# Optimization experiments

Hardware: AMD Instinct MI355X
Metric: run time of the kernel (lower is better)

The kernel has to match this reference:

```python
import jax, jax.numpy as jnp
import numpy as np

H = 64
NUM_LAYERS = 2


def _edge_norm(si, ti, n_s, n_t):
    # per-edge sqrt(deg_src * deg_tgt), degrees counted over this edge type
    ds = jnp.zeros((n_s,), jnp.float32).at[si].add(1.0)
    dt = jnp.zeros((n_t,), jnp.float32).at[ti].add(1.0)
    return jnp.sqrt(ds[si] * dt[ti])


def _light_conv(xd, edge_list, div):
    # gather -> per-edge normalize -> scatter-add per edge type, then mean over
    # incoming edge types and ReLU (applied twice in original since ReLU=True;
    # relu is idempotent)
    out = {}
    for (src, tgt, si, ti, norm) in edge_list:
        msg = xd[src][si] / norm[:, None]          # [E, H]
        agg = jnp.zeros_like(xd[tgt]).at[ti].add(msg)
        out[tgt] = out[tgt] + agg if tgt in out else agg
    return {k: jax.nn.relu(v / div[k]) for k, v in out.items()}


def _run_branch(x0, edge_list, div):
    # concat=True: mean over stacked per-layer outputs; initial embeddings are
    # included only for spot and user (as in the original forward)
    all_x = {k: [] for k in x0}
    all_x['spot'].append(x0['spot'])
    all_x['user'].append(x0['user'])
    xd = x0
    for _ in range(NUM_LAYERS):
        xd = _light_conv(xd, edge_list, div)
        for k in xd:
            all_x[k].append(xd[k])
    return {k: jnp.mean(jnp.stack(v, axis=1), axis=1) for k, v in all_x.items()}


def setup_inputs() -> dict:
    key = jax.random.key(0)
    ks = jax.random.split(key, 32)
    NU, NS, NC, NCI, NP = 200000, 50000, 512, 2000, 47
    E_US, E_SC, E_SCI, E_CP = 1000000, 50000, 50000, 2000

    def emb(k, n):
        return 0.1 * jax.random.normal(k, (n, H), dtype=jnp.float32)

    inp = {
        'user1': emb(ks[0], NU), 'spot1': emb(ks[1], NS),
        'user2': emb(ks[2], NU), 'spot2': emb(ks[3], NS), 'cat2': emb(ks[4], NC),
        'user3': emb(ks[5], NU), 'spot3': emb(ks[6], NS),
        'city3': emb(ks[7], NCI), 'pref3': emb(ks[8], NP),
        'user4': emb(ks[9], NU), 'spot4': emb(ks[10], NS),
        'city4': emb(ks[11], NCI), 'pref4': emb(ks[12], NP), 'cat4': emb(ks[13], NC),
        'lin_w_user': 0.0625 * jax.random.normal(ks[14], (4 * H, 1), jnp.float32),
        'lin_b_user': jnp.zeros((1,), jnp.float32),
        'lin_w_spot': 0.0625 * jax.random.normal(ks[15], (4 * H, 1), jnp.float32),
        'lin_b_spot': jnp.zeros((1,), jnp.float32),
        'us_src': jax.random.randint(ks[16], (E_US,), 0, NU, jnp.int32),
        'us_dst': jax.random.randint(ks[17], (E_US,), 0, NS, jnp.int32),
        'sc_src': jax.random.randint(ks[18], (E_SC,), 0, NS, jnp.int32),
        'sc_dst': jax.random.randint(ks[19], (E_SC,), 0, NC, jnp.int32),
        'sci_src': jax.random.randint(ks[20], (E_SCI,), 0, NS, jnp.int32),
        'sci_dst': jax.random.randint(ks[21], (E_SCI,), 0, NCI, jnp.int32),
        'cp_src': jax.random.randint(ks[22], (E_CP,), 0, NCI, jnp.int32),
        'cp_dst': jax.random.randint(ks[23], (E_CP,), 0, NP, jnp.int32),
    }
    return inp


def reference(user1, spot1, user2, spot2, cat2, user3, spot3, city3, pref3,
              user4, spot4, city4, pref4, cat4,
              lin_w_user, lin_b_user, lin_w_spot, lin_b_spot,
              us_src, us_dst, sc_src, sc_dst, sci_src, sci_dst, cp_src, cp_dst):
    NU, NS = user1.shape[0], spot1.shape[0]
    NC, NCI, NP = cat2.shape[0], city3.shape[0], pref3.shape[0]

    n_us = _edge_norm(us_src, us_dst, NU, NS)
    n_sc = _edge_norm(sc_src, sc_dst, NS, NC)
    n_sci = _edge_norm(sci_src, sci_dst, NS, NCI)
    n_cp = _edge_norm(cp_src, cp_dst, NCI, NP)

    us_f = ('user', 'spot', us_src, us_dst, n_us)
    us_r = ('spot', 'user', us_dst, us_src, n_us)
    sc_f = ('spot', 'category', sc_src, sc_dst, n_sc)
    sc_r = ('category', 'spot', sc_dst, sc_src, n_sc)
    sci_f = ('spot', 'city', sci_src, sci_dst, n_sci)
    sci_r = ('city', 'spot', sci_dst, sci_src, n_sci)
    cp_f = ('city', 'pref', cp_src, cp_dst, n_cp)
    cp_r = ('pref', 'city', cp_dst, cp_src, n_cp)

    b1 = _run_branch({'user': user1, 'spot': spot1},
                     [us_f, us_r], {'spot': 1.0, 'user': 1.0})
    b2 = _run_branch({'user': user2, 'spot': spot2, 'category': cat2},
                     [us_f, us_r, sc_f, sc_r],
                     {'spot': 2.0, 'user': 1.0, 'category': 1.0})
    b3 = _run_branch({'user': user3, 'spot': spot3, 'city': city3, 'pref': pref3},
                     [us_f, us_r, sci_f, sci_r, cp_f, cp_r],
                     {'spot': 2.0, 'user': 1.0, 'city': 2.0, 'pref': 1.0})
    b4 = _run_branch({'user': user4, 'spot': spot4, 'city': city4,
                      'pref': pref4, 'category': cat4},
                     [us_f, us_r, sc_f, sc_r, sci_f, sci_r, cp_f, cp_r],
                     {'spot': 3.0, 'user': 1.0, 'city': 2.0, 'pref': 1.0,
                      'category': 1.0})

    xu = jnp.concatenate([b1['user'], b2['user'], b3['user'], b4['user']], axis=1)
    xs = jnp.concatenate([b1['spot'], b2['spot'], b3['spot'], b4['spot']], axis=1)
    user_out = xu @ lin_w_user + lin_b_user   # [NU, 1]
    spot_out = xs @ lin_w_spot + lin_b_spot   # [NS, 1]
    return jnp.concatenate([user_out, spot_out], axis=0)
```

## Files before the change

### kernel.cpp

```cpp
#include <hip/hip_runtime.h>

#define HD 64
#define ROW 256

__device__ inline unsigned short f2bf(float f) {
    unsigned u = __builtin_bit_cast(unsigned, f);
    u += 0x7FFFu + ((u >> 16) & 1u);
    return (unsigned short)(u >> 16);
}
__device__ inline float bf2f(unsigned short h) {
    unsigned u = ((unsigned)h) << 16;
    return __builtin_bit_cast(float, u);
}


__global__ void k_count(const int* __restrict__ s, const int* __restrict__ t, int E,
                        unsigned* __restrict__ ds, unsigned* __restrict__ dt) {
    int i = blockIdx.x * blockDim.x + threadIdx.x;
    int st = gridDim.x * blockDim.x;
    for (; i < E; i += st) {
        atomicAdd(ds + s[i], 1u);
        atomicAdd(dt + t[i], 1u);
    }
}

__global__ void k_rs(const unsigned* __restrict__ d, float* __restrict__ r, int n) {
    int i = blockIdx.x * blockDim.x + threadIdx.x;
    if (i < n) {
        unsigned v = d[i];
        r[i] = v ? 1.0f / sqrtf((float)v) : 0.0f;
    }
}

__global__ void k_off(const unsigned* __restrict__ deg, int n, unsigned* __restrict__ off,
                      unsigned* __restrict__ cur, unsigned* __restrict__ cnt) {
    int i = blockIdx.x * blockDim.x + threadIdx.x;
    if (i < n) {
        unsigned o = atomicAdd(cnt, deg[i]);
        off[i] = o;
        cur[i] = o;
    }
}

__global__ void k_fill(const int* __restrict__ s, const int* __restrict__ t, int E,
                       unsigned* __restrict__ cur, int* __restrict__ col) {
    int i = blockIdx.x * blockDim.x + threadIdx.x;
    int st = gridDim.x * blockDim.x;
    for (; i < E; i += st) {
        int p = (int)atomicAdd(cur + t[i], 1u);
        col[p] = s[i];
    }
}

__global__ void k_sentinel(float* __restrict__ out, int n, float val) {
    int i = blockIdx.x * blockDim.x + threadIdx.x;
    if (i < n) out[i] = val;
}


__global__ void k_l1_user(const int* __restrict__ col, const unsigned* __restrict__ off,
                          const unsigned* __restrict__ deg,
                          const float* __restrict__ rs_src, const float* __restrict__ rs_dst,
                          const float* __restrict__ s1, const float* __restrict__ s2,
                          const float* __restrict__ s3, const float* __restrict__ s4,
                          unsigned short* __restrict__ out, int n) {
    int w = (blockIdx.x * blockDim.x + threadIdx.x) >> 6;
    int lane = threadIdx.x & 63;
    if (w >= n) return;
    unsigned o = off[w], d = deg[w];
    float a0 = 0, a1 = 0, a2 = 0, a3 = 0;
    for (unsigned e = 0; e < d; ++e) {
        int s = col[o + e];
        float sc = rs_src[s];
        int b = s * HD + lane;
        a0 = fmaf(s1[b], sc, a0);
        a1 = fmaf(s2[b], sc, a1);
        a2 = fmaf(s3[b], sc, a2);
        a3 = fmaf(s4[b], sc, a3);
    }
    float rd = rs_dst[w];
    ushort4 pk;
    pk.x = f2bf(fmaxf(a0 * rd, 0.f));
    pk.y = f2bf(fmaxf(a1 * rd, 0.f));
    pk.z = f2bf(fmaxf(a2 * rd, 0.f));
    pk.w = f2bf(fmaxf(a3 * rd, 0.f));
    *reinterpret_cast<ushort4*>(out + w * ROW + lane * 4) = pk;
}

__global__ void k_l1_spot(
    const int* __restrict__ colU, const unsigned* __restrict__ offU, const unsigned* __restrict__ degU,
    const float* __restrict__ rsU_src, const float* __restrict__ rsU_dst,
    const int* __restrict__ colC, const unsigned* __restrict__ offC, const unsigned* __restrict__ degC,
    const float* __restrict__ rsC_src, const float* __restrict__ rsC_dst,
    const int* __restrict__ colI, const unsigned* __restrict__ offI, const unsigned* __restrict__ degI,
    const float* __restrict__ rsI_src, const float* __restrict__ rsI_dst,
    const float* __restrict__ u1, const float* __restrict__ u2,
    const float* __restrict__ u3, const float* __restrict__ u4,
    const float* __restrict__ c2, const float* __restrict__ c4,
    const float* __restrict__ i3, const float* __restrict__ i4,
    unsigned short* __restrict__ out, int n) {
    int w = (blockIdx.x * blockDim.x + threadIdx.x) >> 6;
    int lane = threadIdx.x & 63;
    if (w >= n) return;
    float a0 = 0, a1 = 0, a2 = 0, a3 = 0;
    {
        unsigned o = offU[w], d = degU[w];
        for (unsigned e = 0; e < d; ++e) {
            int s = colU[o + e];
            float sc = rsU_src[s];
            int b = s * HD + lane;
            a0 = fmaf(u1[b], sc, a0);
            a1 = fmaf(u2[b], sc, a1);
            a2 = fmaf(u3[b], sc, a2);
            a3 = fmaf(u4[b], sc, a3);
        }
        float rd = rsU_dst[w];
        a0 *= rd; a1 *= rd; a2 *= rd; a3 *= rd;
    }
    float cA = 0, cB = 0;
    {
        unsigned o = offC[w], d = degC[w];
        for (unsigned e = 0; e < d; ++e) {
            int s = colC[o + e];
            float sc = rsC_src[s];
            int b = s * HD + lane;
            cA = fmaf(c2[b], sc, cA);
            cB = fmaf(c4[b], sc, cB);
        }
        float rd = rsC_dst[w];
        cA *= rd; cB *= rd;
    }
    float iA = 0, iB = 0;
    {
        unsigned o = offI[w], d = degI[w];
        for (unsigned e = 0; e < d; ++e) {
            int s = colI[o + e];
            float sc = rsI_src[s];
            int b = s * HD + lane;
            iA = fmaf(i3[b], sc, iA);
            iB = fmaf(i4[b], sc, iB);
        }
        float rd = rsI_dst[w];
        iA *= rd; iB *= rd;
    }
    ushort4 pk;
    pk.x = f2bf(fmaxf(a0, 0.f));
    pk.y = f2bf(fmaxf((a1 + cA) * 0.5f, 0.f));
    pk.z = f2bf(fmaxf((a2 + iA) * 0.5f, 0.f));
    pk.w = f2bf(fmaxf((a3 + cB + iB) * (1.0f / 3.0f), 0.f));
    *reinterpret_cast<ushort4*>(out + w * ROW + lane * 4) = pk;
}

__global__ void k_l1_cat(const int* __restrict__ col, const unsigned* __restrict__ off,
                         const unsigned* __restrict__ deg,
                         const float* __restrict__ rs_src, const float* __restrict__ rs_dst,
                         const float* __restrict__ s2, const float* __restrict__ s4,
                         unsigned short* __restrict__ out, int n) {
    int w = (blockIdx.x * blockDim.x + threadIdx.x) >> 6;
    int lane = threadIdx.x & 63;
    if (w >= n) return;
    unsigned o = off[w], d = deg[w];
    float a1 = 0, a3 = 0;
    for (unsigned e = 0; e < d; ++e) {
        int s = col[o + e];
        float sc = rs_src[s];
        int b = s * HD + lane;
        a1 = fmaf(s2[b], sc, a1);
        a3 = fmaf(s4[b], sc, a3);
    }
    float rd = rs_dst[w];
    ushort4 pk;
    pk.x = 0;
    pk.y = f2bf(fmaxf(a1 * rd, 0.f));
    pk.z = 0;
    pk.w = f2bf(fmaxf(a3 * rd, 0.f));
    *reinterpret_cast<ushort4*>(out + w * ROW + lane * 4) = pk;
}

__global__ void k_l1_city(const int* __restrict__ colS, const unsigned* __restrict__ offS,
                          const unsigned* __restrict__ degS,
                          const float* __restrict__ rsS_src, const float* __restrict__ rsS_dst,
                          const int* __restrict__ colP, const unsigned* __restrict__ offP,
                          const unsigned* __restrict__ degP,
                          const float* __restrict__ rsP_src, const float* __restrict__ rsP_dst,
                          const float* __restrict__ s3, const float* __restrict__ s4,
                          const float* __restrict__ p3, const float* __restrict__ p4,
                          unsigned short* __restrict__ out, int n) {
    int w = (blockIdx.x * blockDim.x + threadIdx.x) >> 6;
    int lane = threadIdx.x & 63;
    if (w >= n) return;
    float a2 = 0, a3 = 0;
    {
        unsigned o = offS[w], d = degS[w];
        for (unsigned e = 0; e < d; ++e) {
            int s = colS[o + e];
            float sc = rsS_src[s];
            int b = s * HD + lane;
            a2 = fmaf(s3[b], sc, a2);
            a3 = fmaf(s4[b], sc, a3);
        }
        float rd = rsS_dst[w];
        a2 *= rd; a3 *= rd;
    }
    float b2 = 0, b3 = 0;
    {
        unsigned o = offP[w], d = degP[w];
        for (unsigned e = 0; e < d; ++e) {
            int s = colP[o + e];
            float sc = rsP_src[s];
            int b = s * HD + lane;
            b2 = fmaf(p3[b], sc, b2);
            b3 = fmaf(p4[b], sc, b3);
        }
        float rd = rsP_dst[w];
        b2 *= rd; b3 *= rd;
    }
    ushort4 pk;
    pk.x = 0;
    pk.y = 0;
    pk.z = f2bf(fmaxf((a2 + b2) * 0.5f, 0.f));
    pk.w = f2bf(fmaxf((a3 + b3) * 0.5f, 0.f));
    *reinterpret_cast<ushort4*>(out + w * ROW + lane * 4) = pk;
}


__global__ void k_user_out(const int* __restrict__ col, const unsigned* __restrict__ off,
                           const unsigned* __restrict__ deg,
                           const float* __restrict__ rs_src, const float* __restrict__ rs_dst,
                           const unsigned short* __restrict__ l1spot,
                           const unsigned short* __restrict__ l1user,
                           const float* __restrict__ x1, const float* __restrict__ x2,
                           const float* __restrict__ x3, const float* __restrict__ x4,
                           const float* __restrict__ wlin, const float* __restrict__ blin,
                           float* __restrict__ out, int n) {
    int u = (blockIdx.x * blockDim.x + threadIdx.x) >> 6;
    int lane = threadIdx.x & 63;
    if (u >= n) return;
    float a0 = 0, a1 = 0, a2 = 0, a3 = 0;
    unsigned o = off[u], d = deg[u];
    for (unsigned e = 0; e < d; ++e) {
        int s = col[o + e];
        float sc = rs_src[s];
        ushort4 v = *reinterpret_cast<const ushort4*>(l1spot + s * ROW + lane * 4);
        a0 = fmaf(bf2f(v.x), sc, a0);
        a1 = fmaf(bf2f(v.y), sc, a1);
        a2 = fmaf(bf2f(v.z), sc, a2);
        a3 = fmaf(bf2f(v.w), sc, a3);
    }
    float rd = rs_dst[u];
    a0 = fmaxf(a0 * rd, 0.f);
    a1 = fmaxf(a1 * rd, 0.f);
    a2 = fmaxf(a2 * rd, 0.f);
    a3 = fmaxf(a3 * rd, 0.f);
    int xb = u * HD + lane;
    ushort4 lv = *reinterpret_cast<const ushort4*>(l1user + u * ROW + lane * 4);
    const float third = 1.0f / 3.0f;
    float m0 = (x1[xb] + bf2f(lv.x) + a0) * third;
    float m1 = (x2[xb] + bf2f(lv.y) + a1) * third;
    float m2 = (x3[xb] + bf2f(lv.z) + a2) * third;
    float m3 = (x4[xb] + bf2f(lv.w) + a3) * third;
    float p = m0 * wlin[lane] + m1 * wlin[HD + lane] + m2 * wlin[2 * HD + lane] +
              m3 * wlin[3 * HD + lane];
#pragma unroll
    for (int ofs = 32; ofs; ofs >>= 1) p += __shfl_xor(p, ofs, 64);
    if (lane == 0) out[u] = p + blin[0];
}

__global__ void k_spot_out(
    const int* __restrict__ colU, const unsigned* __restrict__ offU, const unsigned* __restrict__ degU,
    const float* __restrict__ rsU_src, const float* __restrict__ rsU_dst,
    const int* __restrict__ colC, const unsigned* __restrict__ offC, const unsigned* __restrict__ degC,
    const float* __restrict__ rsC_src, const float* __restrict__ rsC_dst,
    const int* __restrict__ colI, const unsigned* __restrict__ offI, const unsigned* __restrict__ degI,
    const float* __restrict__ rsI_src, const float* __restrict__ rsI_dst,
    const unsigned short* __restrict__ l1user, const unsigned short* __restrict__ l1cat,
    const unsigned short* __restrict__ l1city, const unsigned short* __restrict__ l1spot,
    const float* __restrict__ x1, const float* __restrict__ x2,
    const float* __restrict__ x3, const float* __restrict__ x4,
    const float* __restrict__ wlin, const float* __restrict__ blin,
    float* __restrict__ out, int n) {
    int w = (blockIdx.x * blockDim.x + threadIdx.x) >> 6;
    int lane = threadIdx.x & 63;
    if (w >= n) return;
    float a0 = 0, a1 = 0, a2 = 0, a3 = 0;
    {
        unsigned o = offU[w], d = degU[w];
        for (unsigned e = 0; e < d; ++e) {
            int s = colU[o + e];
            float sc = rsU_src[s];
            ushort4 v = *reinterpret_cast<const ushort4*>(l1user + s * ROW + lane * 4);
            a0 = fmaf(bf2f(v.x), sc, a0);
            a1 = fmaf(bf2f(v.y), sc, a1);
            a2 = fmaf(bf2f(v.z), sc, a2);
            a3 = fmaf(bf2f(v.w), sc, a3);
        }
        float rd = rsU_dst[w];
        a0 *= rd; a1 *= rd; a2 *= rd; a3 *= rd;
    }
    float cA = 0, cB = 0;
    {
        unsigned o = offC[w], d = degC[w];
        for (unsigned e = 0; e < d; ++e) {
            int s = colC[o + e];
            float sc = rsC_src[s];
            ushort4 v = *reinterpret_cast<const ushort4*>(l1cat + s * ROW + lane * 4);
            cA = fmaf(bf2f(v.y), sc, cA);
            cB = fmaf(bf2f(v.w), sc, cB);
        }
        float rd = rsC_dst[w];
        cA *= rd; cB *= rd;
    }
    float iA = 0, iB = 0;
    {
        unsigned o = offI[w], d = degI[w];
        for (unsigned e = 0; e < d; ++e) {
            int s = colI[o + e];
            float sc = rsI_src[s];
            ushort4 v = *reinterpret_cast<const ushort4*>(l1city + s * ROW + lane * 4);
            iA = fmaf(bf2f(v.z), sc, iA);
            iB = fmaf(bf2f(v.w), sc, iB);
        }
        float rd = rsI_dst[w];
        iA *= rd; iB *= rd;
    }
    float L0 = fmaxf(a0, 0.f);
    float L1 = fmaxf((a1 + cA) * 0.5f, 0.f);
    float L2 = fmaxf((a2 + iA) * 0.5f, 0.f);
    float L3 = fmaxf((a3 + cB + iB) * (1.0f / 3.0f), 0.f);
    int xb = w * HD + lane;
    ushort4 lv = *reinterpret_cast<const ushort4*>(l1spot + w * ROW + lane * 4);
    const float third = 1.0f / 3.0f;
    float m0 = (x1[xb] + bf2f(lv.x) + L0) * third;
    float m1 = (x2[xb] + bf2f(lv.y) + L1) * third;
    float m2 = (x3[xb] + bf2f(lv.z) + L2) * third;
    float m3 = (x4[xb] + bf2f(lv.w) + L3) * third;
    float p = m0 * wlin[lane] + m1 * wlin[HD + lane] + m2 * wlin[2 * HD + lane] +
              m3 * wlin[3 * HD + lane];
#pragma unroll
    for (int ofs = 32; ofs; ofs >>= 1) p += __shfl_xor(p, ofs, 64);
    if (lane == 0) out[w] = p + blin[0];
}


static inline unsigned cdivu(unsigned a, unsigned b) { return (a + b - 1) / b; }

extern "C" void kernel_launch(void* const* d_in, const int* in_sizes, int n_in,
                              void* d_out, int out_size, void* d_ws, size_t ws_size,
                              hipStream_t stream) {
    const float* user1 = (const float*)d_in[0];
    const float* spot1 = (const float*)d_in[1];
    const float* user2 = (const float*)d_in[2];
    const float* spot2 = (const float*)d_in[3];
    const float* cat2  = (const float*)d_in[4];
    const float* user3 = (const float*)d_in[5];
    const float* spot3 = (const float*)d_in[6];
    const float* city3 = (const float*)d_in[7];
    const float* pref3 = (const float*)d_in[8];
    const float* user4 = (const float*)d_in[9];
    const float* spot4 = (const float*)d_in[10];
    const float* city4 = (const float*)d_in[11];
    const float* pref4 = (const float*)d_in[12];
    const float* cat4  = (const float*)d_in[13];
    const float* w_user = (const float*)d_in[14];
    const float* b_user = (const float*)d_in[15];
    const float* w_spot = (const float*)d_in[16];
    const float* b_spot = (const float*)d_in[17];
    const int* us_src  = (const int*)d_in[18];
    const int* us_dst  = (const int*)d_in[19];
    const int* sc_src  = (const int*)d_in[20];
    const int* sc_dst  = (const int*)d_in[21];
    const int* sci_src = (const int*)d_in[22];
    const int* sci_dst = (const int*)d_in[23];
    const int* cp_src  = (const int*)d_in[24];
    const int* cp_dst  = (const int*)d_in[25];

    const int NU = in_sizes[0] / HD, NS = in_sizes[1] / HD, NC = in_sizes[4] / HD;
    const int NCI = in_sizes[7] / HD, NP = in_sizes[8] / HD;
    const int EUS = in_sizes[18], ESC = in_sizes[20], ESCI = in_sizes[22], ECP = in_sizes[24];

    char* wp = (char*)d_ws;
    auto alloc = [&](size_t bytes) -> void* {
        void* r = (void*)wp;
        wp += (bytes + 255) & ~(size_t)255;
        return r;
    };

    const size_t nDeg = (size_t)NU + NS + NS + NC + NS + NCI + NCI + NP;
    unsigned* degBase = (unsigned*)alloc((nDeg + 8) * sizeof(unsigned));
    unsigned* ds_u   = degBase;
    unsigned* dt_s   = ds_u + NU;
    unsigned* ds_ssc = dt_s + NS;
    unsigned* dt_c   = ds_ssc + NS;
    unsigned* ds_ssi = dt_c + NC;
    unsigned* dt_ci  = ds_ssi + NS;
    unsigned* ds_cic = dt_ci + NCI;
    unsigned* dt_p   = ds_cic + NCI;
    unsigned* cnt    = dt_p + NP;

    float* rsBase = (float*)alloc(nDeg * sizeof(float));
    float* rs_ds_u   = rsBase;
    float* rs_dt_s   = rs_ds_u + NU;
    float* rs_ds_ssc = rs_dt_s + NS;
    float* rs_dt_c   = rs_ds_ssc + NS;
    float* rs_ds_ssi = rs_dt_c + NC;
    float* rs_dt_ci  = rs_ds_ssi + NS;
    float* rs_ds_cic = rs_dt_ci + NCI;
    float* rs_dt_p   = rs_ds_cic + NCI;

    unsigned* off_usf = (unsigned*)alloc(NS * 4);  unsigned* cur_usf = (unsigned*)alloc(NS * 4);
    unsigned* off_usr = (unsigned*)alloc((size_t)NU * 4); unsigned* cur_usr = (unsigned*)alloc((size_t)NU * 4);
    unsigned* off_scf = (unsigned*)alloc(NC * 4);  unsigned* cur_scf = (unsigned*)alloc(NC * 4);
    unsigned* off_scr = (unsigned*)alloc(NS * 4);  unsigned* cur_scr = (unsigned*)alloc(NS * 4);
    unsigned* off_sif = (unsigned*)alloc(NCI * 4); unsigned* cur_sif = (unsigned*)alloc(NCI * 4);
    unsigned* off_sir = (unsigned*)alloc(NS * 4);  unsigned* cur_sir = (unsigned*)alloc(NS * 4);
    unsigned* off_cpr = (unsigned*)alloc(NCI * 4); unsigned* cur_cpr = (unsigned*)alloc(NCI * 4);
    int* col_usf = (int*)alloc((size_t)EUS * 4);
    int* col_usr = (int*)alloc((size_t)EUS * 4);
    int* col_scf = (int*)alloc((size_t)ESC * 4);
    int* col_scr = (int*)alloc((size_t)ESC * 4);
    int* col_sif = (int*)alloc((size_t)ESCI * 4);
    int* col_sir = (int*)alloc((size_t)ESCI * 4);
    int* col_cpr = (int*)alloc((size_t)ECP * 4);

    unsigned short* l1_user = (unsigned short*)alloc((size_t)NU * ROW * 2);
    unsigned short* l1_spot = (unsigned short*)alloc((size_t)NS * ROW * 2);
    unsigned short* l1_cat  = (unsigned short*)alloc((size_t)NC * ROW * 2);
    unsigned short* l1_city = (unsigned short*)alloc((size_t)NCI * ROW * 2);

    float* outU = (float*)d_out;
    float* outS = outU + NU;

    size_t need = (size_t)(wp - (char*)d_ws);
    if (need > ws_size) {
        float val = 1000.0f + (float)(ws_size >> 20);
        k_sentinel<<<cdivu((unsigned)out_size, 256), 256, 0, stream>>>((float*)d_out, out_size, val);
        return;
    }

    hipMemsetAsync(degBase, 0, (nDeg + 8) * sizeof(unsigned), stream);
    k_count<<<1024, 256, 0, stream>>>(us_src, us_dst, EUS, ds_u, dt_s);
    k_count<<<256, 256, 0, stream>>>(sc_src, sc_dst, ESC, ds_ssc, dt_c);
    k_count<<<256, 256, 0, stream>>>(sci_src, sci_dst, ESCI, ds_ssi, dt_ci);
    k_count<<<32, 256, 0, stream>>>(cp_src, cp_dst, ECP, ds_cic, dt_p);
    k_rs<<<cdivu((unsigned)nDeg, 256), 256, 0, stream>>>(degBase, rsBase, (int)nDeg);

    k_off<<<cdivu(NS, 256), 256, 0, stream>>>(dt_s, NS, off_usf, cur_usf, cnt + 0);
    k_off<<<cdivu(NU, 256), 256, 0, stream>>>(ds_u, NU, off_usr, cur_usr, cnt + 1);
    k_off<<<cdivu(NC, 256), 256, 0, stream>>>(dt_c, NC, off_scf, cur_scf, cnt + 2);
    k_off<<<cdivu(NS, 256), 256, 0, stream>>>(ds_ssc, NS, off_scr, cur_scr, cnt + 3);
    k_off<<<cdivu(NCI, 256), 256, 0, stream>>>(dt_ci, NCI, off_sif, cur_sif, cnt + 4);
    k_off<<<cdivu(NS, 256), 256, 0, stream>>>(ds_ssi, NS, off_sir, cur_sir, cnt + 5);
    k_off<<<cdivu(NCI, 256), 256, 0, stream>>>(ds_cic, NCI, off_cpr, cur_cpr, cnt + 6);

    k_fill<<<1024, 256, 0, stream>>>(us_src, us_dst, EUS, cur_usf, col_usf);
    k_fill<<<1024, 256, 0, stream>>>(us_dst, us_src, EUS, cur_usr, col_usr);
    k_fill<<<256, 256, 0, stream>>>(sc_src, sc_dst, ESC, cur_scf, col_scf);
    k_fill<<<256, 256, 0, stream>>>(sc_dst, sc_src, ESC, cur_scr, col_scr);
    k_fill<<<256, 256, 0, stream>>>(sci_src, sci_dst, ESCI, cur_sif, col_sif);
    k_fill<<<256, 256, 0, stream>>>(sci_dst, sci_src, ESCI, cur_sir, col_sir);
    k_fill<<<32, 256, 0, stream>>>(cp_dst, cp_src, ECP, cur_cpr, col_cpr);

    k_l1_user<<<cdivu(NU, 4), 256, 0, stream>>>(
        col_usr, off_usr, ds_u, rs_dt_s, rs_ds_u,
        spot1, spot2, spot3, spot4, l1_user, NU);
    k_l1_spot<<<cdivu(NS, 4), 256, 0, stream>>>(
        col_usf, off_usf, dt_s, rs_ds_u, rs_dt_s,
        col_scr, off_scr, ds_ssc, rs_dt_c, rs_ds_ssc,
        col_sir, off_sir, ds_ssi, rs_dt_ci, rs_ds_ssi,
        user1, user2, user3, user4, cat2, cat4, city3, city4, l1_spot, NS);
    k_l1_cat<<<cdivu(NC, 4), 256, 0, stream>>>(
        col_scf, off_scf, dt_c, rs_ds_ssc, rs_dt_c, spot2, spot4, l1_cat, NC);
    k_l1_city<<<cdivu(NCI, 4), 256, 0, stream>>>(
        col_sif, off_sif, dt_ci, rs_ds_ssi, rs_dt_ci,
        col_cpr, off_cpr, ds_cic, rs_dt_p, rs_ds_cic,
        spot3, spot4, pref3, pref4, l1_city, NCI);

    k_user_out<<<cdivu(NU, 4), 256, 0, stream>>>(
        col_usr, off_usr, ds_u, rs_dt_s, rs_ds_u,
        l1_spot, l1_user, user1, user2, user3, user4,
        w_user, b_user, outU, NU);
    k_spot_out<<<cdivu(NS, 4), 256, 0, stream>>>(
        col_usf, off_usf, dt_s, rs_ds_u, rs_dt_s,
        col_scr, off_scr, ds_ssc, rs_dt_c, rs_ds_ssc,
        col_sir, off_sir, ds_ssi, rs_dt_ci, rs_ds_ssi,
        l1_user, l1_cat, l1_city, l1_spot,
        spot1, spot2, spot3, spot4,
        w_spot, b_spot, outS, NS);

    (void)n_in; (void)out_size; (void)ws_size; (void)NP;
}
```

Measured before the change: 1.415 ms.

## Pre-pack layer-0 embeddings into interleaved fp16 rows and switch intermediates to fp16

```diff
diff --git a/kernel.cpp b/kernel.cpp
--- a/kernel.cpp
+++ b/kernel.cpp
@@ -3,15 +3,8 @@
 #define HD 64
 #define ROW 256
 
-__device__ inline unsigned short f2bf(float f) {
-    unsigned u = __builtin_bit_cast(unsigned, f);
-    u += 0x7FFFu + ((u >> 16) & 1u);
-    return (unsigned short)(u >> 16);
-}
-__device__ inline float bf2f(unsigned short h) {
-    unsigned u = ((unsigned)h) << 16;
-    return __builtin_bit_cast(float, u);
-}
+typedef _Float16 h16;
+typedef __attribute__((ext_vector_type(4))) _Float16 h16x4;
 
 
 __global__ void k_count(const int* __restrict__ s, const int* __restrict__ t, int E,
@@ -58,12 +51,65 @@
 }
 
 
+__global__ void k_pack4_scaled(const float* __restrict__ a, const float* __restrict__ b,
+                               const float* __restrict__ c, const float* __restrict__ d,
+                               const float* __restrict__ rs, h16* __restrict__ out, int nElem) {
+    int i = blockIdx.x * blockDim.x + threadIdx.x;
+    if (i >= nElem) return;
+    float sc = rs[i >> 6];
+    h16x4 pk;
+    pk.x = (h16)(a[i] * sc);
+    pk.y = (h16)(b[i] * sc);
+    pk.z = (h16)(c[i] * sc);
+    pk.w = (h16)(d[i] * sc);
+    *reinterpret_cast<h16x4*>(out + ((size_t)i << 2)) = pk;
+}
+
+__global__ void k_pack4_plain(const float* __restrict__ a, const float* __restrict__ b,
+                              const float* __restrict__ c, const float* __restrict__ d,
+                              h16* __restrict__ out, int nElem) {
+    int i = blockIdx.x * blockDim.x + threadIdx.x;
+    if (i >= nElem) return;
+    h16x4 pk;
+    pk.x = (h16)a[i];
+    pk.y = (h16)b[i];
+    pk.z = (h16)c[i];
+    pk.w = (h16)d[i];
+    *reinterpret_cast<h16x4*>(out + ((size_t)i << 2)) = pk;
+}
+
+__global__ void k_pack2_13_scaled(const float* __restrict__ b, const float* __restrict__ d,
+                                  const float* __restrict__ rs, h16* __restrict__ out, int nElem) {
+    int i = blockIdx.x * blockDim.x + threadIdx.x;
+    if (i >= nElem) return;
+    float sc = rs[i >> 6];
+    h16x4 pk;
+    pk.x = (h16)0.f;
+    pk.y = (h16)(b[i] * sc);
+    pk.z = (h16)0.f;
+    pk.w = (h16)(d[i] * sc);
+    *reinterpret_cast<h16x4*>(out + ((size_t)i << 2)) = pk;
+}
+
+__global__ void k_pack2_23_scaled(const float* __restrict__ c, const float* __restrict__ d,
+                                  const float* __restrict__ rs, h16* __restrict__ out, int nElem) {
+    int i = blockIdx.x * blockDim.x + threadIdx.x;
+    if (i >= nElem) return;
+    float sc = rs[i >> 6];
+    h16x4 pk;
+    pk.x = (h16)0.f;
+    pk.y = (h16)0.f;
+    pk.z = (h16)(c[i] * sc);
+    pk.w = (h16)(d[i] * sc);
+    *reinterpret_cast<h16x4*>(out + ((size_t)i << 2)) = pk;
+}
+
+
 __global__ void k_l1_user(const int* __restrict__ col, const unsigned* __restrict__ off,
                           const unsigned* __restrict__ deg,
                           const float* __restrict__ rs_src, const float* __restrict__ rs_dst,
-                          const float* __restrict__ s1, const float* __restrict__ s2,
-                          const float* __restrict__ s3, const float* __restrict__ s4,
-                          unsigned short* __restrict__ out, int n) {
+                          const h16* __restrict__ pkS,
+                          h16* __restrict__ out, int n) {
     int w = (blockIdx.x * blockDim.x + threadIdx.x) >> 6;
     int lane = threadIdx.x & 63;
     if (w >= n) return;
@@ -72,33 +118,30 @@
     for (unsigned e = 0; e < d; ++e) {
         int s = col[o + e];
         float sc = rs_src[s];
-        int b = s * HD + lane;
-        a0 = fmaf(s1[b], sc, a0);
-        a1 = fmaf(s2[b], sc, a1);
-        a2 = fmaf(s3[b], sc, a2);
-        a3 = fmaf(s4[b], sc, a3);
+        h16x4 v = *reinterpret_cast<const h16x4*>(pkS + s * ROW + lane * 4);
+        a0 = fmaf((float)v.x, sc, a0);
+        a1 = fmaf((float)v.y, sc, a1);
+        a2 = fmaf((float)v.z, sc, a2);
+        a3 = fmaf((float)v.w, sc, a3);
     }
     float rd = rs_dst[w];
-    ushort4 pk;
-    pk.x = f2bf(fmaxf(a0 * rd, 0.f));
-    pk.y = f2bf(fmaxf(a1 * rd, 0.f));
-    pk.z = f2bf(fmaxf(a2 * rd, 0.f));
-    pk.w = f2bf(fmaxf(a3 * rd, 0.f));
-    *reinterpret_cast<ushort4*>(out + w * ROW + lane * 4) = pk;
+    h16x4 pk;
+    pk.x = (h16)fmaxf(a0 * rd, 0.f);
+    pk.y = (h16)fmaxf(a1 * rd, 0.f);
+    pk.z = (h16)fmaxf(a2 * rd, 0.f);
+    pk.w = (h16)fmaxf(a3 * rd, 0.f);
+    *reinterpret_cast<h16x4*>(out + w * ROW + lane * 4) = pk;
 }
 
 __global__ void k_l1_spot(
     const int* __restrict__ colU, const unsigned* __restrict__ offU, const unsigned* __restrict__ degU,
-    const float* __restrict__ rsU_src, const float* __restrict__ rsU_dst,
+    const float* __restrict__ rsU_dst,
     const int* __restrict__ colC, const unsigned* __restrict__ offC, const unsigned* __restrict__ degC,
-    const float* __restrict__ rsC_src, const float* __restrict__ rsC_dst,
+    const float* __restrict__ rsC_dst,
     const int* __restrict__ colI, const unsigned* __restrict__ offI, const unsigned* __restrict__ degI,
-    const float* __restrict__ rsI_src, const float* __restrict__ rsI_dst,
-    const float* __restrict__ u1, const float* __restrict__ u2,
-    const float* __restrict__ u3, const float* __restrict__ u4,
-    const float* __restrict__ c2, const float* __restrict__ c4,
-    const float* __restrict__ i3, const float* __restrict__ i4,
-    unsigned short* __restrict__ out, int n) {
+    const float* __restrict__ rsI_dst,
+    const h16* __restrict__ pkU, const h16* __restrict__ pkC, const h16* __restrict__ pkI,
+    h16* __restrict__ out, int n) {
     int w = (blockIdx.x * blockDim.x + threadIdx.x) >> 6;
     int lane = threadIdx.x & 63;
     if (w >= n) return;
@@ -107,12 +150,11 @@
         unsigned o = offU[w], d = degU[w];
         for (unsigned e = 0; e < d; ++e) {
             int s = colU[o + e];
-            float sc = rsU_src[s];
-            int b = s * HD + lane;
-            a0 = fmaf(u1[b], sc, a0);
-            a1 = fmaf(u2[b], sc, a1);
-            a2 = fmaf(u3[b], sc, a2);
-            a3 = fmaf(u4[b], sc, a3);
+            h16x4 v = *reinterpret_cast<const h16x4*>(pkU + s * ROW + lane * 4);
+            a0 += (float)v.x;
+            a1 += (float)v.y;
+            a2 += (float)v.z;
+            a3 += (float)v.w;
         }
         float rd = rsU_dst[w];
         a0 *= rd; a1 *= rd; a2 *= rd; a3 *= rd;
@@ -122,10 +164,9 @@
         unsigned o = offC[w], d = degC[w];
         for (unsigned e = 0; e < d; ++e) {
             int s = colC[o + e];
-            float sc = rsC_src[s];
-            int b = s * HD + lane;
-            cA = fmaf(c2[b], sc, cA);
-            cB = fmaf(c4[b], sc, cB);
+            h16x4 v = *reinterpret_cast<const h16x4*>(pkC + s * ROW + lane * 4);
+            cA += (float)v.y;
+            cB += (float)v.w;
         }
         float rd = rsC_dst[w];
         cA *= rd; cB *= rd;
@@ -135,27 +176,26 @@
         unsigned o = offI[w], d = degI[w];
         for (unsigned e = 0; e < d; ++e) {
             int s = colI[o + e];
-            float sc = rsI_src[s];
-            int b = s * HD + lane;
-            iA = fmaf(i3[b], sc, iA);
-            iB = fmaf(i4[b], sc, iB);
+            h16x4 v = *reinterpret_cast<const h16x4*>(pkI + s * ROW + lane * 4);
+            iA += (float)v.z;
+            iB += (float)v.w;
         }
         float rd = rsI_dst[w];
         iA *= rd; iB *= rd;
     }
-    ushort4 pk;
-    pk.x = f2bf(fmaxf(a0, 0.f));
-    pk.y = f2bf(fmaxf((a1 + cA) * 0.5f, 0.f));
-    pk.z = f2bf(fmaxf((a2 + iA) * 0.5f, 0.f));
-    pk.w = f2bf(fmaxf((a3 + cB + iB) * (1.0f / 3.0f), 0.f));
-    *reinterpret_cast<ushort4*>(out + w * ROW + lane * 4) = pk;
+    h16x4 pk;
+    pk.x = (h16)fmaxf(a0, 0.f);
+    pk.y = (h16)fmaxf((a1 + cA) * 0.5f, 0.f);
+    pk.z = (h16)fmaxf((a2 + iA) * 0.5f, 0.f);
+    pk.w = (h16)fmaxf((a3 + cB + iB) * (1.0f / 3.0f), 0.f);
+    *reinterpret_cast<h16x4*>(out + w * ROW + lane * 4) = pk;
 }
 
 __global__ void k_l1_cat(const int* __restrict__ col, const unsigned* __restrict__ off,
                          const unsigned* __restrict__ deg,
                          const float* __restrict__ rs_src, const float* __restrict__ rs_dst,
-                         const float* __restrict__ s2, const float* __restrict__ s4,
-                         unsigned short* __restrict__ out, int n) {
+                         const h16* __restrict__ pkS,
+                         h16* __restrict__ out, int n) {
     int w = (blockIdx.x * blockDim.x + threadIdx.x) >> 6;
     int lane = threadIdx.x & 63;
     if (w >= n) return;
@@ -164,17 +204,17 @@
     for (unsigned e = 0; e < d; ++e) {
         int s = col[o + e];
         float sc = rs_src[s];
-        int b = s * HD + lane;
-        a1 = fmaf(s2[b], sc, a1);
-        a3 = fmaf(s4[b], sc, a3);
+        h16x4 v = *reinterpret_cast<const h16x4*>(pkS + s * ROW + lane * 4);
+        a1 = fmaf((float)v.y, sc, a1);
+        a3 = fmaf((float)v.w, sc, a3);
     }
     float rd = rs_dst[w];
-    ushort4 pk;
-    pk.x = 0;
-    pk.y = f2bf(fmaxf(a1 * rd, 0.f));
-    pk.z = 0;
-    pk.w = f2bf(fmaxf(a3 * rd, 0.f));
-    *reinterpret_cast<ushort4*>(out + w * ROW + lane * 4) = pk;
+    h16x4 pk;
+    pk.x = (h16)0.f;
+    pk.y = (h16)fmaxf(a1 * rd, 0.f);
+    pk.z = (h16)0.f;
+    pk.w = (h16)fmaxf(a3 * rd, 0.f);
+    *reinterpret_cast<h16x4*>(out + w * ROW + lane * 4) = pk;
 }
 
 __global__ void k_l1_city(const int* __restrict__ colS, const unsigned* __restrict__ offS,
@@ -182,10 +222,9 @@
                           const float* __restrict__ rsS_src, const float* __restrict__ rsS_dst,
                           const int* __restrict__ colP, const unsigned* __restrict__ offP,
                           const unsigned* __restrict__ degP,
-                          const float* __restrict__ rsP_src, const float* __restrict__ rsP_dst,
-                          const float* __restrict__ s3, const float* __restrict__ s4,
-                          const float* __restrict__ p3, const float* __restrict__ p4,
-                          unsigned short* __restrict__ out, int n) {
+                          const float* __restrict__ rsP_dst,
+                          const h16* __restrict__ pkS, const h16* __restrict__ pkP,
+                          h16* __restrict__ out, int n) {
     int w = (blockIdx.x * blockDim.x + threadIdx.x) >> 6;
     int lane = threadIdx.x & 63;
     if (w >= n) return;
@@ -195,9 +234,9 @@
         for (unsigned e = 0; e < d; ++e) {
             int s = colS[o + e];
             float sc = rsS_src[s];
-            int b = s * HD + lane;
-            a2 = fmaf(s3[b], sc, a2);
-            a3 = fmaf(s4[b], sc, a3);
+            h16x4 v = *reinterpret_cast<const h16x4*>(pkS + s * ROW + lane * 4);
+            a2 = fmaf((float)v.z, sc, a2);
+            a3 = fmaf((float)v.w, sc, a3);
         }
         float rd = rsS_dst[w];
         a2 *= rd; a3 *= rd;
@@ -207,28 +246,26 @@
         unsigned o = offP[w], d = degP[w];
         for (unsigned e = 0; e < d; ++e) {
             int s = colP[o + e];
-            float sc = rsP_src[s];
-            int b = s * HD + lane;
-            b2 = fmaf(p3[b], sc, b2);
-            b3 = fmaf(p4[b], sc, b3);
+            h16x4 v = *reinterpret_cast<const h16x4*>(pkP + s * ROW + lane * 4);
+            b2 += (float)v.z;
+            b3 += (float)v.w;
         }
         float rd = rsP_dst[w];
         b2 *= rd; b3 *= rd;
     }
-    ushort4 pk;
-    pk.x = 0;
-    pk.y = 0;
-    pk.z = f2bf(fmaxf((a2 + b2) * 0.5f, 0.f));
-    pk.w = f2bf(fmaxf((a3 + b3) * 0.5f, 0.f));
-    *reinterpret_cast<ushort4*>(out + w * ROW + lane * 4) = pk;
+    h16x4 pk;
+    pk.x = (h16)0.f;
+    pk.y = (h16)0.f;
+    pk.z = (h16)fmaxf((a2 + b2) * 0.5f, 0.f);
+    pk.w = (h16)fmaxf((a3 + b3) * 0.5f, 0.f);
+    *reinterpret_cast<h16x4*>(out + w * ROW + lane * 4) = pk;
 }
 
 
 __global__ void k_user_out(const int* __restrict__ col, const unsigned* __restrict__ off,
                            const unsigned* __restrict__ deg,
                            const float* __restrict__ rs_src, const float* __restrict__ rs_dst,
-                           const unsigned short* __restrict__ l1spot,
-                           const unsigned short* __restrict__ l1user,
+                           const h16* __restrict__ l1spot, const h16* __restrict__ l1user,
                            const float* __restrict__ x1, const float* __restrict__ x2,
                            const float* __restrict__ x3, const float* __restrict__ x4,
                            const float* __restrict__ wlin, const float* __restrict__ blin,
@@ -241,11 +278,11 @@
     for (unsigned e = 0; e < d; ++e) {
         int s = col[o + e];
         float sc = rs_src[s];
-        ushort4 v = *reinterpret_cast<const ushort4*>(l1spot + s * ROW + lane * 4);
-        a0 = fmaf(bf2f(v.x), sc, a0);
-        a1 = fmaf(bf2f(v.y), sc, a1);
-        a2 = fmaf(bf2f(v.z), sc, a2);
-        a3 = fmaf(bf2f(v.w), sc, a3);
+        h16x4 v = *reinterpret_cast<const h16x4*>(l1spot + s * ROW + lane * 4);
+        a0 = fmaf((float)v.x, sc, a0);
+        a1 = fmaf((float)v.y, sc, a1);
+        a2 = fmaf((float)v.z, sc, a2);
+        a3 = fmaf((float)v.w, sc, a3);
     }
     float rd = rs_dst[u];
     a0 = fmaxf(a0 * rd, 0.f);
@@ -253,12 +290,12 @@
     a2 = fmaxf(a2 * rd, 0.f);
     a3 = fmaxf(a3 * rd, 0.f);
     int xb = u * HD + lane;
-    ushort4 lv = *reinterpret_cast<const ushort4*>(l1user + u * ROW + lane * 4);
+    h16x4 lv = *reinterpret_cast<const h16x4*>(l1user + u * ROW + lane * 4);
     const float third = 1.0f / 3.0f;
-    float m0 = (x1[xb] + bf2f(lv.x) + a0) * third;
-    float m1 = (x2[xb] + bf2f(lv.y) + a1) * third;
-    float m2 = (x3[xb] + bf2f(lv.z) + a2) * third;
-    float m3 = (x4[xb] + bf2f(lv.w) + a3) * third;
+    float m0 = (x1[xb] + (float)lv.x + a0) * third;
+    float m1 = (x2[xb] + (float)lv.y + a1) * third;
+    float m2 = (x3[xb] + (float)lv.z + a2) * third;
+    float m3 = (x4[xb] + (float)lv.w + a3) * third;
     float p = m0 * wlin[lane] + m1 * wlin[HD + lane] + m2 * wlin[2 * HD + lane] +
               m3 * wlin[3 * HD + lane];
 #pragma unroll
@@ -273,8 +310,8 @@
     const float* __restrict__ rsC_src, const float* __restrict__ rsC_dst,
     const int* __restrict__ colI, const unsigned* __restrict__ offI, const unsigned* __restrict__ degI,
     const float* __restrict__ rsI_src, const float* __restrict__ rsI_dst,
-    const unsigned short* __restrict__ l1user, const unsigned short* __restrict__ l1cat,
-    const unsigned short* __restrict__ l1city, const unsigned short* __restrict__ l1spot,
+    const h16* __restrict__ l1user, const h16* __restrict__ l1cat,
+    const h16* __restrict__ l1city, const h16* __restrict__ l1spot,
     const float* __restrict__ x1, const float* __restrict__ x2,
     const float* __restrict__ x3, const float* __restrict__ x4,
     const float* __restrict__ wlin, const float* __restrict__ blin,
@@ -288,11 +325,11 @@
         for (unsigned e = 0; e < d; ++e) {
             int s = colU[o + e];
             float sc = rsU_src[s];
-            ushort4 v = *reinterpret_cast<const ushort4*>(l1user + s * ROW + lane * 4);
-            a0 = fmaf(bf2f(v.x), sc, a0);
-            a1 = fmaf(bf2f(v.y), sc, a1);
-            a2 = fmaf(bf2f(v.z), sc, a2);
-            a3 = fmaf(bf2f(v.w), sc, a3);
+            h16x4 v = *reinterpret_cast<const h16x4*>(l1user + s * ROW + lane * 4);
+            a0 = fmaf((float)v.x, sc, a0);
+            a1 = fmaf((float)v.y, sc, a1);
+            a2 = fmaf((float)v.z, sc, a2);
+            a3 = fmaf((float)v.w, sc, a3);
         }
         float rd = rsU_dst[w];
         a0 *= rd; a1 *= rd; a2 *= rd; a3 *= rd;
@@ -303,9 +340,9 @@
         for (unsigned e = 0; e < d; ++e) {
             int s = colC[o + e];
             float sc = rsC_src[s];
-            ushort4 v = *reinterpret_cast<const ushort4*>(l1cat + s * ROW + lane * 4);
-            cA = fmaf(bf2f(v.y), sc, cA);
-            cB = fmaf(bf2f(v.w), sc, cB);
+            h16x4 v = *reinterpret_cast<const h16x4*>(l1cat + s * ROW + lane * 4);
+            cA = fmaf((float)v.y, sc, cA);
+            cB = fmaf((float)v.w, sc, cB);
         }
         float rd = rsC_dst[w];
         cA *= rd; cB *= rd;
@@ -316,9 +353,9 @@
         for (unsigned e = 0; e < d; ++e) {
             int s = colI[o + e];
             float sc = rsI_src[s];
-            ushort4 v = *reinterpret_cast<const ushort4*>(l1city + s * ROW + lane * 4);
-            iA = fmaf(bf2f(v.z), sc, iA);
-            iB = fmaf(bf2f(v.w), sc, iB);
+            h16x4 v = *reinterpret_cast<const h16x4*>(l1city + s * ROW + lane * 4);
+            iA = fmaf((float)v.z, sc, iA);
+            iB = fmaf((float)v.w, sc, iB);
         }
         float rd = rsI_dst[w];
         iA *= rd; iB *= rd;
@@ -328,12 +365,12 @@
     float L2 = fmaxf((a2 + iA) * 0.5f, 0.f);
     float L3 = fmaxf((a3 + cB + iB) * (1.0f / 3.0f), 0.f);
     int xb = w * HD + lane;
-    ushort4 lv = *reinterpret_cast<const ushort4*>(l1spot + w * ROW + lane * 4);
+    h16x4 lv = *reinterpret_cast<const h16x4*>(l1spot + w * ROW + lane * 4);
     const float third = 1.0f / 3.0f;
-    float m0 = (x1[xb] + bf2f(lv.x) + L0) * third;
-    float m1 = (x2[xb] + bf2f(lv.y) + L1) * third;
-    float m2 = (x3[xb] + bf2f(lv.z) + L2) * third;
-    float m3 = (x4[xb] + bf2f(lv.w) + L3) * third;
+    float m0 = (x1[xb] + (float)lv.x + L0) * third;
+    float m1 = (x2[xb] + (float)lv.y + L1) * third;
+    float m2 = (x3[xb] + (float)lv.z + L2) * third;
+    float m3 = (x4[xb] + (float)lv.w + L3) * third;
     float p = m0 * wlin[lane] + m1 * wlin[HD + lane] + m2 * wlin[2 * HD + lane] +
               m3 * wlin[3 * HD + lane];
 #pragma unroll
@@ -422,10 +459,16 @@
     int* col_sir = (int*)alloc((size_t)ESCI * 4);
     int* col_cpr = (int*)alloc((size_t)ECP * 4);
 
-    unsigned short* l1_user = (unsigned short*)alloc((size_t)NU * ROW * 2);
-    unsigned short* l1_spot = (unsigned short*)alloc((size_t)NS * ROW * 2);
-    unsigned short* l1_cat  = (unsigned short*)alloc((size_t)NC * ROW * 2);
-    unsigned short* l1_city = (unsigned short*)alloc((size_t)NCI * ROW * 2);
+    h16* pk_user = (h16*)alloc((size_t)NU * ROW * 2);
+    h16* pk_spot = (h16*)alloc((size_t)NS * ROW * 2);
+    h16* pk_cat  = (h16*)alloc((size_t)NC * ROW * 2);
+    h16* pk_city = (h16*)alloc((size_t)NCI * ROW * 2);
+    h16* pk_pref = (h16*)alloc((size_t)NP * ROW * 2);
+
+    h16* l1_user = pk_user;
+    h16* l1_spot = (h16*)alloc((size_t)NS * ROW * 2);
+    h16* l1_cat  = (h16*)alloc((size_t)NC * ROW * 2);
+    h16* l1_city = (h16*)alloc((size_t)NCI * ROW * 2);
 
     float* outU = (float*)d_out;
     float* outS = outU + NU;
@@ -460,20 +503,31 @@
     k_fill<<<256, 256, 0, stream>>>(sci_dst, sci_src, ESCI, cur_sir, col_sir);
     k_fill<<<32, 256, 0, stream>>>(cp_dst, cp_src, ECP, cur_cpr, col_cpr);
 
+    k_pack4_scaled<<<cdivu(NU * HD, 256), 256, 0, stream>>>(
+        user1, user2, user3, user4, rs_ds_u, pk_user, NU * HD);
+    k_pack4_plain<<<cdivu(NS * HD, 256), 256, 0, stream>>>(
+        spot1, spot2, spot3, spot4, pk_spot, NS * HD);
+    k_pack2_13_scaled<<<cdivu(NC * HD, 256), 256, 0, stream>>>(
+        cat2, cat4, rs_dt_c, pk_cat, NC * HD);
+    k_pack2_23_scaled<<<cdivu(NCI * HD, 256), 256, 0, stream>>>(
+        city3, city4, rs_dt_ci, pk_city, NCI * HD);
+    k_pack2_23_scaled<<<cdivu(NP * HD, 256), 256, 0, stream>>>(
+        pref3, pref4, rs_dt_p, pk_pref, NP * HD);
+
+    k_l1_spot<<<cdivu(NS, 4), 256, 0, stream>>>(
+        col_usf, off_usf, dt_s, rs_dt_s,
+        col_scr, off_scr, ds_ssc, rs_ds_ssc,
+        col_sir, off_sir, ds_ssi, rs_ds_ssi,
+        pk_user, pk_cat, pk_city, l1_spot, NS);
+    k_l1_cat<<<cdivu(NC, 4), 256, 0, stream>>>(
+        col_scf, off_scf, dt_c, rs_ds_ssc, rs_dt_c, pk_spot, l1_cat, NC);
+    k_l1_city<<<cdivu(NCI, 4), 256, 0, stream>>>(
+        col_sif, off_sif, dt_ci, rs_ds_ssi, rs_dt_ci,
+        col_cpr, off_cpr, ds_cic, rs_ds_cic,
+        pk_spot, pk_pref, l1_city, NCI);
     k_l1_user<<<cdivu(NU, 4), 256, 0, stream>>>(
         col_usr, off_usr, ds_u, rs_dt_s, rs_ds_u,
-        spot1, spot2, spot3, spot4, l1_user, NU);
-    k_l1_spot<<<cdivu(NS, 4), 256, 0, stream>>>(
-        col_usf, off_usf, dt_s, rs_ds_u, rs_dt_s,
-        col_scr, off_scr, ds_ssc, rs_dt_c, rs_ds_ssc,
-        col_sir, off_sir, ds_ssi, rs_dt_ci, rs_ds_ssi,
-        user1, user2, user3, user4, cat2, cat4, city3, city4, l1_spot, NS);
-    k_l1_cat<<<cdivu(NC, 4), 256, 0, stream>>>(
-        col_scf, off_scf, dt_c, rs_ds_ssc, rs_dt_c, spot2, spot4, l1_cat, NC);
-    k_l1_city<<<cdivu(NCI, 4), 256, 0, stream>>>(
-        col_sif, off_sif, dt_ci, rs_ds_ssi, rs_dt_ci,
-        col_cpr, off_cpr, ds_cic, rs_dt_p, rs_ds_cic,
-        spot3, spot4, pref3, pref4, l1_city, NCI);
+        pk_spot, l1_user, NU);
 
     k_user_out<<<cdivu(NU, 4), 256, 0, stream>>>(
         col_usr, off_usr, ds_u, rs_dt_s, rs_ds_u,
```

Measured after the change: 1.406 ms. About the same (-0.7%).
